# Performance work log

Hardware: AMD Instinct MI355X
Metric: run time of the kernel (lower is better)

Reference implementation:

```python
import jax, jax.numpy as jnp
import numpy as np
import math

B, L, D_MODEL, H = 2, 2048, 2048, 16
HD = D_MODEL // H  # 128


def _rope(x):
    # x: (B,H,L,HD) interleaved-pair RoPE (GPT-NeoX / RoFormer style with ::2 strides)
    hd = x.shape[-1]
    inv_freq = 1.0 / (10000.0 ** (jnp.arange(0, hd, 2, dtype=jnp.float32) / hd))  # (HD/2,)
    t = jnp.arange(x.shape[2], dtype=jnp.float32)
    freqs = t[:, None] * inv_freq[None, :]            # (L, HD/2)
    cos = jnp.cos(freqs)[None, None]                  # (1,1,L,HD/2)
    sin = jnp.sin(freqs)[None, None]
    x1 = x[..., ::2]
    x2 = x[..., 1::2]
    even = x1 * cos - x2 * sin
    odd = x1 * sin + x2 * cos
    # interleave even/odd back: (...,HD/2,2) -> (...,HD)
    return jnp.stack([even, odd], axis=-1).reshape(x.shape)


def setup_inputs() -> dict:
    key = jax.random.key(0)
    k1, k2, k3, k4, k5, k6 = jax.random.split(key, 6)
    x_q = jax.random.normal(k1, (B, L, D_MODEL), dtype=jnp.float32)
    x_kv = jax.random.normal(k2, (B, L, D_MODEL), dtype=jnp.float32)
    # causal additive mask: 0 keep, -1e9 masked, broadcastable to (B,H,L,S)
    causal = jnp.tril(jnp.ones((L, L), dtype=bool))
    attn_mask = jnp.where(causal, 0.0, -1e9).astype(jnp.float32)[None, None]
    s = 0.02
    w_q = jax.random.normal(k3, (D_MODEL, D_MODEL), dtype=jnp.float32) * s
    w_k = jax.random.normal(k4, (D_MODEL, D_MODEL), dtype=jnp.float32) * s
    w_v = jax.random.normal(k5, (D_MODEL, D_MODEL), dtype=jnp.float32) * s
    w_o = jax.random.normal(k6, (D_MODEL, D_MODEL), dtype=jnp.float32) * s
    return {"x_q": x_q, "x_kv": x_kv, "attn_mask": attn_mask,
            "w_q": w_q, "w_k": w_k, "w_v": w_v, "w_o": w_o}


def _shape(x):
    b, l, _ = x.shape
    return x.reshape(b, l, H, HD).transpose(0, 2, 1, 3)  # (B,H,L,HD)


def reference(x_q, x_kv, attn_mask, w_q, w_k, w_v, w_o):
    # torch Linear (no bias): y = x @ W.T
    q = _shape(x_q @ w_q.T)
    k = _shape(x_kv @ w_k.T)
    v = _shape(x_kv @ w_v.T)
    q = _rope(q)
    k = _rope(k)
    scale = 1.0 / math.sqrt(HD)
    scores = jnp.einsum('bhld,bhsd->bhls', q, k) * scale + attn_mask
    attn = jax.nn.softmax(scores, axis=-1)            # (B,H,L,S)
    out = jnp.einsum('bhls,bhsd->bhld', attn, v)
    out = out.transpose(0, 2, 1, 3).reshape(x_q.shape[0], x_q.shape[1], H * HD)
    out = out @ w_o.T
    return (out, attn)
```

## Files before the change

### kernel.cpp

```cpp
#include <hip/hip_runtime.h>
#include <hip/hip_bf16.h>
#include <math.h>

#define B_ 2
#define L_ 2048
#define D_ 2048
#define H_ 16
#define HD_ 128
#define E_ (B_*L_*D_)
#define W_ (D_*D_)

typedef __bf16 bf16;
typedef __bf16 bf16x8 __attribute__((ext_vector_type(8)));
typedef __bf16 bf16x4 __attribute__((ext_vector_type(4)));
typedef float  f32x4  __attribute__((ext_vector_type(4)));

#define GLL16(gp_, lp_) __builtin_amdgcn_global_load_lds( \
    (const __attribute__((address_space(1))) void*)(gp_), \
    (__attribute__((address_space(3))) void*)(lp_), 16, 0, 0)

#define BARRIER() do { asm volatile("" ::: "memory"); \
    __builtin_amdgcn_s_barrier(); \
    asm volatile("" ::: "memory"); } while (0)

#define WAITN(N) asm volatile("s_waitcnt vmcnt(" #N ")" ::: "memory")

__global__ void cvt2(const float* __restrict__ s0, const float* __restrict__ s1,
                     bf16* __restrict__ d0, bf16* __restrict__ d1, int n) {
  const float* s = blockIdx.y ? s1 : s0;
  bf16* d = blockIdx.y ? d1 : d0;
  int i = (blockIdx.x * blockDim.x + threadIdx.x) * 4;
  if (i + 3 < n) {
    f32x4 v = *reinterpret_cast<const f32x4*>(s + i);
    bf16x4 o;
    o[0] = (bf16)v[0]; o[1] = (bf16)v[1]; o[2] = (bf16)v[2]; o[3] = (bf16)v[3];
    *reinterpret_cast<bf16x4*>(d + i) = o;
  }
}
__global__ void cvt4(const float* __restrict__ s0, const float* __restrict__ s1,
                     const float* __restrict__ s2, const float* __restrict__ s3,
                     bf16* __restrict__ d0, bf16* __restrict__ d1,
                     bf16* __restrict__ d2, bf16* __restrict__ d3, int n) {
  const float* s; bf16* d;
  switch (blockIdx.y) {
    case 0: s = s0; d = d0; break;
    case 1: s = s1; d = d1; break;
    case 2: s = s2; d = d2; break;
    default: s = s3; d = d3; break;
  }
  int i = (blockIdx.x * blockDim.x + threadIdx.x) * 4;
  if (i + 3 < n) {
    f32x4 v = *reinterpret_cast<const f32x4*>(s + i);
    bf16x4 o;
    o[0] = (bf16)v[0]; o[1] = (bf16)v[1]; o[2] = (bf16)v[2]; o[3] = (bf16)v[3];
    *reinterpret_cast<bf16x4*>(d + i) = o;
  }
}

__global__ void rope_table(float* __restrict__ ct, float* __restrict__ st) {
  int t = blockIdx.x;
  int i = threadIdx.x;
  float inv = powf(10000.0f, -2.0f * (float)i / 128.0f);
  float f = (float)t * inv;
  ct[t * 64 + i] = cosf(f);
  st[t * 64 + i] = sinf(f);
}

__global__ void rope_inplace(bf16* __restrict__ Q, bf16* __restrict__ Kt,
                             const float* __restrict__ ct, const float* __restrict__ st) {
  size_t idx = (size_t)blockIdx.x * blockDim.x + threadIdx.x;
  const size_t per = E_ / 8;
  bf16* P = (idx < per) ? Q : Kt;
  size_t li = ((idx < per) ? idx : idx - per) * 8;
  int l   = (int)((li / D_) % L_);
  int col = (int)(li % D_);
  int i0  = (col & 127) >> 1;
  bf16x8 v = *reinterpret_cast<const bf16x8*>(P + li);
  f32x4 c4 = *reinterpret_cast<const f32x4*>(ct + l * 64 + i0);
  f32x4 s4 = *reinterpret_cast<const f32x4*>(st + l * 64 + i0);
  bf16x8 o;
#pragma unroll
  for (int p = 0; p < 4; ++p) {
    float x1 = (float)v[2*p], x2 = (float)v[2*p+1];
    o[2*p]   = (bf16)(x1 * c4[p] - x2 * s4[p]);
    o[2*p+1] = (bf16)(x1 * s4[p] + x2 * c4[p]);
  }
  *reinterpret_cast<bf16x8*>(P + li) = o;
}

__global__ void transpose_v(const bf16* __restrict__ Vraw, bf16* __restrict__ Vt) {
  __shared__ bf16 tile[32][33];
  int bh = blockIdx.z; int b = bh >> 4, h = bh & 15;
  int l0 = blockIdx.x * 32, d0 = blockIdx.y * 32;
  int tx = threadIdx.x, ty = threadIdx.y;
#pragma unroll
  for (int j = 0; j < 4; ++j) {
    int r = ty + j * 8;
    tile[r][tx] = Vraw[((size_t)b * L_ + l0 + r) * D_ + h * HD_ + d0 + tx];
  }
  __syncthreads();
#pragma unroll
  for (int j = 0; j < 4; ++j) {
    int r = ty + j * 8;
    Vt[((size_t)bh * HD_ + d0 + r) * L_ + l0 + tx] = tile[tx][r];
  }
}

template<int OUT_BF16>
__global__ __launch_bounds__(256, 4) void gemm_bt(const bf16* __restrict__ A,
                                                  const bf16* __restrict__ Bw,
                                                  void* __restrict__ Cout,
                                                  int M, int N, int K) {
  __shared__ bf16 As[128 * 64];
  __shared__ bf16 Bs[128 * 64];
  const int tid = threadIdx.x;
  const int lane = tid & 63;
  const int w = tid >> 6;
  const int l15 = lane & 15, lg = lane >> 4;
  const int m0 = blockIdx.y * 128, n0 = blockIdx.x * 128;
  const int wm = (w >> 1) * 64, wn = (w & 1) * 64;

  int rowS[4], schS[4];
#pragma unroll
  for (int s = 0; s < 4; ++s) {
    int cl = s * 256 + tid;
    rowS[s] = cl >> 3;
    schS[s] = ((cl & 7) ^ ((cl >> 3) & 7)) << 3;
  }

  f32x4 acc[4][4];
#pragma unroll
  for (int m = 0; m < 4; ++m)
#pragma unroll
    for (int n = 0; n < 4; ++n) acc[m][n] = (f32x4){0.f, 0.f, 0.f, 0.f};

  for (int kt = 0; kt < K; kt += 64) {
    __syncthreads();
#pragma unroll
    for (int s = 0; s < 4; ++s) {
      GLL16(A  + (size_t)(m0 + rowS[s]) * K + kt + schS[s], As + s * 2048 + w * 512);
      GLL16(Bw + (size_t)(n0 + rowS[s]) * K + kt + schS[s], Bs + s * 2048 + w * 512);
    }
    __syncthreads();
#pragma unroll
    for (int kk = 0; kk < 64; kk += 32) {
      bf16x8 af[4], bfr[4];
#pragma unroll
      for (int m = 0; m < 4; ++m)
        af[m] = *reinterpret_cast<const bf16x8*>(
            As + (wm + m * 16 + l15) * 64 + ((((kk >> 3) + lg) ^ (l15 & 7)) << 3));
#pragma unroll
      for (int n = 0; n < 4; ++n)
        bfr[n] = *reinterpret_cast<const bf16x8*>(
            Bs + (wn + n * 16 + l15) * 64 + ((((kk >> 3) + lg) ^ (l15 & 7)) << 3));
#pragma unroll
      for (int m = 0; m < 4; ++m)
#pragma unroll
        for (int n = 0; n < 4; ++n)
          acc[m][n] = __builtin_amdgcn_mfma_f32_16x16x32_bf16(af[m], bfr[n], acc[m][n], 0, 0, 0);
    }
  }
#pragma unroll
  for (int m = 0; m < 4; ++m) {
    int orow = m0 + wm + m * 16 + lg * 4;
#pragma unroll
    for (int n = 0; n < 4; ++n) {
      int col = n0 + wn + n * 16 + l15;
#pragma unroll
      for (int r = 0; r < 4; ++r) {
        if (OUT_BF16) ((bf16*)Cout)[(size_t)(orow + r) * N + col] = (bf16)acc[m][n][r];
        else          ((float*)Cout)[(size_t)(orow + r) * N + col] = acc[m][n][r];
      }
    }
  }
}

__global__ __launch_bounds__(512, 4) void attn_fused(const bf16* __restrict__ Qb,
                                                     const bf16* __restrict__ Kb,
                                                     const bf16* __restrict__ Vt,
                                                     float* __restrict__ attn,
                                                     bf16* __restrict__ Oh) {
  __shared__ bf16 Klds[2][64 * 128];
  __shared__ bf16 Vlds[128 * 64];
  __shared__ bf16 Plds[8][16][72];

  const int tid = threadIdx.x;
  const int w = tid >> 6, lane = tid & 63;
  const int l15 = lane & 15, lg = lane >> 4;

  int g = blockIdx.x + 16 * blockIdx.y;
  int x, bh;
  if (g < 256) { x = g & 15;        bh = g >> 4; }
  else { int h2 = g - 256; x = 15 - (h2 & 15); bh = 16 + (h2 >> 4); }
  const int b = bh >> 4, h = bh & 15;

  const int qt = (w < 4) ? x : (31 - x);
  const int q0w = qt * 64 + (w & 3) * 16;
  const int ntW = qt + 1;
  const int ntB = 32 - x;
  const float sc2 = 0.08838834764831845f * 1.44269504088896f;

  const bf16* kb = Kb + ((size_t)b * L_) * D_ + h * HD_;
  const bf16* vb = Vt + (size_t)bh * HD_ * L_;
  float* arow = attn + ((size_t)bh * L_ + q0w) * L_;

  bf16x8 qf[4];
  {
    const bf16* qrow = Qb + ((size_t)b * L_ + q0w + l15) * D_ + h * HD_;
#pragma unroll
    for (int c = 0; c < 4; ++c)
      qf[c] = *reinterpret_cast<const bf16x8*>(qrow + c * 32 + lg * 8);
  }

  const int t1 = 512 + tid;
  const int rK0 = tid >> 4, sK0 = ((tid & 15) ^ (rK0 & 7)) << 3;
  const int rK1 = t1 >> 4,  sK1 = ((t1 & 15) ^ (rK1 & 7)) << 3;
  const int rV0 = tid >> 3, sV0 = ((tid & 7) ^ (rV0 & 7)) << 3;
  const int rV1 = t1 >> 3,  sV1 = ((t1 & 7) ^ (rV1 & 7)) << 3;
  bf16* ldsK0 = &Klds[0][0] + w * 512;
  bf16* ldsK1 = &Klds[0][0] + 4096 + w * 512;
  bf16* ldsV0 = Vlds + w * 512;
  bf16* ldsV1 = Vlds + 4096 + w * 512;

  auto stageK = [&](int gp, int buf) {
    GLL16(kb + (size_t)(gp * 64 + rK0) * D_ + sK0, ldsK0 + buf * 8192);
    GLL16(kb + (size_t)(gp * 64 + rK1) * D_ + sK1, ldsK1 + buf * 8192);
  };
  auto stageV = [&](int gp) {
    GLL16(vb + (size_t)rV0 * L_ + gp * 64 + sV0, ldsV0);
    GLL16(vb + (size_t)rV1 * L_ + gp * 64 + sV1, ldsV1);
  };
  auto qkt = [&](const bf16* kl, f32x4* acc) {
#pragma unroll
    for (int c = 0; c < 4; ++c)
#pragma unroll
      for (int t = 0; t < 4; ++t) {
        bf16x8 kf = *reinterpret_cast<const bf16x8*>(
            kl + (t * 16 + l15) * 128 + ((((c << 2) + lg) ^ (l15 & 7)) << 3));
        acc[t] = __builtin_amdgcn_mfma_f32_16x16x32_bf16(qf[c], kf, acc[t], 0, 0, 0);
      }
  };

  float sum[4] = {0.f, 0.f, 0.f, 0.f};
  stageK(0, 0);
  for (int gp = 0; gp < ntB; ++gp) {
    BARRIER();
    const bool hn = (gp + 1 < ntB);
    if (hn) stageK(gp + 1, (gp + 1) & 1);
    const bool pz = (gp > 0) && ((gp - 1) >= ntW);
    if (pz) { if (hn) WAITN(18); else WAITN(16); }
    else    { if (hn) WAITN(2);  else WAITN(0);  }
    BARRIER();
    if (gp < ntW) {
      f32x4 acc[4] = {(f32x4){0,0,0,0},(f32x4){0,0,0,0},(f32x4){0,0,0,0},(f32x4){0,0,0,0}};
      qkt(&Klds[gp & 1][0], acc);
      if (gp < qt) {
#pragma unroll
        for (int t = 0; t < 4; ++t)
#pragma unroll
          for (int r = 0; r < 4; ++r)
            sum[r] += exp2f(acc[t][r] * sc2);
      } else {
#pragma unroll
        for (int t = 0; t < 4; ++t)
#pragma unroll
          for (int r = 0; r < 4; ++r) {
            int kc = gp * 64 + t * 16 + l15;
            int qr = q0w + lg * 4 + r;
            sum[r] += (kc <= qr) ? exp2f(acc[t][r] * sc2) : 0.f;
          }
      }
    } else {
#pragma unroll
      for (int t = 0; t < 4; ++t)
#pragma unroll
        for (int r = 0; r < 4; ++r)
          arow[(size_t)(lg * 4 + r) * L_ + gp * 64 + t * 16 + l15] = 0.f;
    }
  }
#pragma unroll
  for (int r = 0; r < 4; ++r) {
#pragma unroll
    for (int sh = 1; sh < 16; sh <<= 1)
      sum[r] += __shfl_xor(sum[r], sh, 64);
  }
  float rinv[4];
#pragma unroll
  for (int r = 0; r < 4; ++r) rinv[r] = 1.0f / sum[r];

  f32x4 oacc[8];
#pragma unroll
  for (int i = 0; i < 8; ++i) oacc[i] = (f32x4){0.f, 0.f, 0.f, 0.f};

  BARRIER();
  stageK(0, 0);
  for (int gp = 0; gp < ntB; ++gp) {
    BARRIER();
    stageV(gp);
    const bool hn = (gp + 1 < ntB);
    if (hn) stageK(gp + 1, (gp + 1) & 1);
    const bool ps = (gp > 0) && ((gp - 1) < ntW);
    if (ps) { if (hn) WAITN(20); else WAITN(18); }
    else    { if (hn) WAITN(4);  else WAITN(2);  }
    BARRIER();
    const bool act = gp < ntW;
    float pv[4][4];
    if (act) {
      f32x4 acc[4] = {(f32x4){0,0,0,0},(f32x4){0,0,0,0},(f32x4){0,0,0,0},(f32x4){0,0,0,0}};
      qkt(&Klds[gp & 1][0], acc);
      if (gp < qt) {
#pragma unroll
        for (int t = 0; t < 4; ++t)
#pragma unroll
          for (int r = 0; r < 4; ++r)
            pv[t][r] = exp2f(acc[t][r] * sc2) * rinv[r];
      } else {
#pragma unroll
        for (int t = 0; t < 4; ++t)
#pragma unroll
          for (int r = 0; r < 4; ++r) {
            int kc = gp * 64 + t * 16 + l15;
            int qr = q0w + lg * 4 + r;
            pv[t][r] = (kc <= qr) ? exp2f(acc[t][r] * sc2) * rinv[r] : 0.f;
          }
      }
#pragma unroll
      for (int t = 0; t < 4; ++t)
#pragma unroll
        for (int r = 0; r < 4; ++r)
          Plds[w][lg * 4 + r][t * 16 + l15] = (bf16)pv[t][r];
    }
    if (hn) WAITN(2); else WAITN(0);
    if (act) {
#pragma unroll
      for (int t = 0; t < 4; ++t)
#pragma unroll
        for (int r = 0; r < 4; ++r)
          arow[(size_t)(lg * 4 + r) * L_ + gp * 64 + t * 16 + l15] = pv[t][r];
    }
    BARRIER();
    if (act) {
      asm volatile("s_waitcnt lgkmcnt(0)" ::: "memory");
      __builtin_amdgcn_sched_barrier(0);
#pragma unroll
      for (int ck = 0; ck < 2; ++ck) {
        bf16x8 pa = *reinterpret_cast<const bf16x8*>(&Plds[w][l15][ck * 32 + lg * 8]);
#pragma unroll
        for (int t8 = 0; t8 < 8; ++t8) {
          bf16x8 vf = *reinterpret_cast<const bf16x8*>(
              Vlds + (t8 * 16 + l15) * 64 + ((((ck << 2) + lg) ^ (l15 & 7)) << 3));
          oacc[t8] = __builtin_amdgcn_mfma_f32_16x16x32_bf16(pa, vf, oacc[t8], 0, 0, 0);
        }
      }
      asm volatile("s_waitcnt lgkmcnt(0)" ::: "memory");
    }
  }

  for (int gp2 = ntB; gp2 < 32; ++gp2) {
#pragma unroll
    for (int it = 0; it < 4; ++it)
      *reinterpret_cast<f32x4*>(arow + (size_t)l15 * L_ + gp2 * 64 + lg * 4 + it * 16)
          = (f32x4){0.f, 0.f, 0.f, 0.f};
  }

  bf16* orow = Oh + ((size_t)b * L_ + q0w) * D_ + h * HD_;
#pragma unroll
  for (int t8 = 0; t8 < 8; ++t8)
#pragma unroll
    for (int r = 0; r < 4; ++r)
      orow[(size_t)(lg * 4 + r) * D_ + t8 * 16 + l15] = (bf16)oacc[t8][r];
}

extern "C" void kernel_launch(void* const* d_in, const int* in_sizes, int n_in,
                              void* d_out, int out_size, void* d_ws, size_t ws_size,
                              hipStream_t stream) {
  const float* x_q  = (const float*)d_in[0];
  const float* x_kv = (const float*)d_in[1];
  const float* w_q = (const float*)d_in[3];
  const float* w_k = (const float*)d_in[4];
  const float* w_v = (const float*)d_in[5];
  const float* w_o = (const float*)d_in[6];

  char* p = (char*)d_ws;
  auto alloc = [&](size_t bytes) { char* r = p; p += (bytes + 255) & ~(size_t)255; return r; };
  bf16* xq_b  = (bf16*)alloc((size_t)E_ * 2);
  bf16* xkv_b = (bf16*)alloc((size_t)E_ * 2);
  bf16* wq_b  = (bf16*)alloc((size_t)W_ * 2);
  bf16* wk_b  = (bf16*)alloc((size_t)W_ * 2);
  bf16* wv_b  = (bf16*)alloc((size_t)W_ * 2);
  bf16* wo_b  = (bf16*)alloc((size_t)W_ * 2);
  bf16* Qraw  = (bf16*)alloc((size_t)E_ * 2);
  bf16* Kraw  = (bf16*)alloc((size_t)E_ * 2);
  bf16* Vraw  = (bf16*)alloc((size_t)E_ * 2);
  bf16* Vt    = (bf16*)alloc((size_t)E_ * 2);
  bf16* Oh    = (bf16*)alloc((size_t)E_ * 2);
  float* ct   = (float*)alloc((size_t)L_ * 64 * 4);
  float* st2  = (float*)alloc((size_t)L_ * 64 * 4);

  float* out0     = (float*)d_out;
  float* attn_out = out0 + E_;

  cvt2<<<dim3(8192, 2), 256, 0, stream>>>(x_q, x_kv, xq_b, xkv_b, E_);
  cvt4<<<dim3(4096, 4), 256, 0, stream>>>(w_q, w_k, w_v, w_o, wq_b, wk_b, wv_b, wo_b, W_);
  rope_table<<<L_, 64, 0, stream>>>(ct, st2);

  gemm_bt<1><<<dim3(16, 32), 256, 0, stream>>>(xq_b,  wq_b, Qraw, B_*L_, D_, D_);
  gemm_bt<1><<<dim3(16, 32), 256, 0, stream>>>(xkv_b, wk_b, Kraw, B_*L_, D_, D_);
  gemm_bt<1><<<dim3(16, 32), 256, 0, stream>>>(xkv_b, wv_b, Vraw, B_*L_, D_, D_);

  rope_inplace<<<8192, 256, 0, stream>>>(Qraw, Kraw, ct, st2);
  transpose_v<<<dim3(64, 4, 32), dim3(32, 8), 0, stream>>>(Vraw, Vt);
  attn_fused<<<dim3(16, 32), 512, 0, stream>>>(Qraw, Kraw, Vt, attn_out, Oh);
  gemm_bt<0><<<dim3(16, 32), 256, 0, stream>>>(Oh, wo_b, out0, B_*L_, D_, D_);
}
```

Baseline: 477.5 us.

## Fuse QKV projections with RoPE and V-transpose epilogues; merge prep kernels

```diff
diff --git a/kernel.cpp b/kernel.cpp
--- a/kernel.cpp
+++ b/kernel.cpp
@@ -25,91 +25,143 @@
 
 #define WAITN(N) asm volatile("s_waitcnt vmcnt(" #N ")" ::: "memory")
 
-__global__ void cvt2(const float* __restrict__ s0, const float* __restrict__ s1,
-                     bf16* __restrict__ d0, bf16* __restrict__ d1, int n) {
-  const float* s = blockIdx.y ? s1 : s0;
-  bf16* d = blockIdx.y ? d1 : d0;
-  int i = (blockIdx.x * blockDim.x + threadIdx.x) * 4;
-  if (i + 3 < n) {
+__global__ void prep(const float* __restrict__ xq, const float* __restrict__ xkv,
+                     const float* __restrict__ wq, const float* __restrict__ wk,
+                     const float* __restrict__ wv, const float* __restrict__ wo,
+                     bf16* __restrict__ xqb, bf16* __restrict__ xkvb,
+                     bf16* __restrict__ wqb, bf16* __restrict__ wkb,
+                     bf16* __restrict__ wvb, bf16* __restrict__ wob,
+                     float* __restrict__ ct, float* __restrict__ st) {
+  int g = blockIdx.x;
+  if (g < 16384) {
+    const float* s = (g < 8192) ? xq : xkv;
+    bf16* d = (g < 8192) ? xqb : xkvb;
+    int i = ((g & 8191) * 256 + threadIdx.x) * 4;
     f32x4 v = *reinterpret_cast<const f32x4*>(s + i);
-    bf16x4 o;
-    o[0] = (bf16)v[0]; o[1] = (bf16)v[1]; o[2] = (bf16)v[2]; o[3] = (bf16)v[3];
+    bf16x4 o; o[0]=(bf16)v[0]; o[1]=(bf16)v[1]; o[2]=(bf16)v[2]; o[3]=(bf16)v[3];
     *reinterpret_cast<bf16x4*>(d + i) = o;
+  } else if (g < 32768) {
+    int gg = g - 16384;
+    int which = gg >> 12;
+    const float* s = (which==0)?wq:(which==1)?wk:(which==2)?wv:wo;
+    bf16* d = (which==0)?wqb:(which==1)?wkb:(which==2)?wvb:wob;
+    int i = ((gg & 4095) * 256 + threadIdx.x) * 4;
+    f32x4 v = *reinterpret_cast<const f32x4*>(s + i);
+    bf16x4 o; o[0]=(bf16)v[0]; o[1]=(bf16)v[1]; o[2]=(bf16)v[2]; o[3]=(bf16)v[3];
+    *reinterpret_cast<bf16x4*>(d + i) = o;
+  } else {
+    int idx = (g - 32768) * 256 + threadIdx.x;
+    int t = idx >> 6, i = idx & 63;
+    float inv = powf(10000.0f, -2.0f * (float)i / 128.0f);
+    float f = (float)t * inv;
+    ct[t * 64 + i] = cosf(f);
+    st[t * 64 + i] = sinf(f);
   }
 }
-__global__ void cvt4(const float* __restrict__ s0, const float* __restrict__ s1,
-                     const float* __restrict__ s2, const float* __restrict__ s3,
-                     bf16* __restrict__ d0, bf16* __restrict__ d1,
-                     bf16* __restrict__ d2, bf16* __restrict__ d3, int n) {
-  const float* s; bf16* d;
-  switch (blockIdx.y) {
-    case 0: s = s0; d = d0; break;
-    case 1: s = s1; d = d1; break;
-    case 2: s = s2; d = d2; break;
-    default: s = s3; d = d3; break;
-  }
-  int i = (blockIdx.x * blockDim.x + threadIdx.x) * 4;
-  if (i + 3 < n) {
-    f32x4 v = *reinterpret_cast<const f32x4*>(s + i);
-    bf16x4 o;
-    o[0] = (bf16)v[0]; o[1] = (bf16)v[1]; o[2] = (bf16)v[2]; o[3] = (bf16)v[3];
-    *reinterpret_cast<bf16x4*>(d + i) = o;
+
+__global__ __launch_bounds__(256, 4) void gemm_qkv(
+    const bf16* __restrict__ xq, const bf16* __restrict__ xkv,
+    const bf16* __restrict__ wq, const bf16* __restrict__ wk, const bf16* __restrict__ wv,
+    const float* __restrict__ ct, const float* __restrict__ st,
+    bf16* __restrict__ Qo, bf16* __restrict__ Ko, bf16* __restrict__ Vt) {
+  __shared__ bf16 As[128 * 64];
+  __shared__ bf16 Bs[128 * 64];
+  const int tid = threadIdx.x;
+  const int lane = tid & 63;
+  const int w = tid >> 6;
+  const int l15 = lane & 15, lg = lane >> 4;
+  const int which = blockIdx.x >> 4;
+  const int n0 = (blockIdx.x & 15) * 128;
+  const int m0 = blockIdx.y * 128;
+  const int wm = (w >> 1) * 64, wn = (w & 1) * 64;
+  const bf16* A  = (which == 0) ? xq : xkv;
+  const bf16* Wt = (which == 0) ? wq : ((which == 1) ? wk : wv);
+
+  int rowS[4], schS[4];
+#pragma unroll
+  for (int s = 0; s < 4; ++s) {
+    int cl = s * 256 + tid;
+    rowS[s] = cl >> 3;
+    schS[s] = ((cl & 7) ^ ((cl >> 3) & 7)) << 3;
+  }
+
+  f32x4 acc[4][4];
+#pragma unroll
+  for (int m = 0; m < 4; ++m)
+#pragma unroll
+    for (int n = 0; n < 4; ++n) acc[m][n] = (f32x4){0.f, 0.f, 0.f, 0.f};
+
+  for (int kt = 0; kt < D_; kt += 64) {
+    __syncthreads();
+#pragma unroll
+    for (int s = 0; s < 4; ++s) {
+      GLL16(A  + (size_t)(m0 + rowS[s]) * D_ + kt + schS[s], As + s * 2048 + w * 512);
+      GLL16(Wt + (size_t)(n0 + rowS[s]) * D_ + kt + schS[s], Bs + s * 2048 + w * 512);
+    }
+    __syncthreads();
+#pragma unroll
+    for (int kk = 0; kk < 64; kk += 32) {
+      bf16x8 af[4], bfr[4];
+#pragma unroll
+      for (int m = 0; m < 4; ++m)
+        af[m] = *reinterpret_cast<const bf16x8*>(
+            As + (wm + m * 16 + l15) * 64 + ((((kk >> 3) + lg) ^ (l15 & 7)) << 3));
+#pragma unroll
+      for (int n = 0; n < 4; ++n)
+        bfr[n] = *reinterpret_cast<const bf16x8*>(
+            Bs + (wn + n * 16 + l15) * 64 + ((((kk >> 3) + lg) ^ (l15 & 7)) << 3));
+#pragma unroll
+      for (int m = 0; m < 4; ++m)
+#pragma unroll
+        for (int n = 0; n < 4; ++n)
+          acc[m][n] = __builtin_amdgcn_mfma_f32_16x16x32_bf16(af[m], bfr[n], acc[m][n], 0, 0, 0);
+    }
+  }
+
+  if (which == 2) {
+    const int b = m0 >> 11;
+    const int l0b = (m0 & 2047) + wm + lg * 4;
+#pragma unroll
+    for (int m = 0; m < 4; ++m) {
+      int l0 = l0b + m * 16;
+#pragma unroll
+      for (int n = 0; n < 4; ++n) {
+        int c = n0 + wn + n * 16 + l15;
+        int hd = (b * 16 + (c >> 7)) * 128 + (c & 127);
+        bf16x4 o;
+        o[0] = (bf16)acc[m][n][0]; o[1] = (bf16)acc[m][n][1];
+        o[2] = (bf16)acc[m][n][2]; o[3] = (bf16)acc[m][n][3];
+        *reinterpret_cast<bf16x4*>(Vt + (size_t)hd * L_ + l0) = o;
+      }
+    }
+  } else {
+    bf16* Out = which ? Ko : Qo;
+    const bool odd = (l15 & 1);
+#pragma unroll
+    for (int m = 0; m < 4; ++m) {
+      int row = m0 + wm + m * 16 + lg * 4;
+      int l = row & 2047;
+#pragma unroll
+      for (int n = 0; n < 4; ++n) {
+        int c = n0 + wn + n * 16 + l15;
+        int i = (c & 127) >> 1;
+#pragma unroll
+        for (int r = 0; r < 4; ++r) {
+          float own = acc[m][n][r];
+          float prt = __shfl_xor(own, 1, 64);
+          float cc = ct[(size_t)(l + r) * 64 + i];
+          float ss = st[(size_t)(l + r) * 64 + i];
+          float res = odd ? (prt * ss + own * cc) : (own * cc - prt * ss);
+          Out[(size_t)(row + r) * D_ + c] = (bf16)res;
+        }
+      }
+    }
   }
 }
 
-__global__ void rope_table(float* __restrict__ ct, float* __restrict__ st) {
-  int t = blockIdx.x;
-  int i = threadIdx.x;
-  float inv = powf(10000.0f, -2.0f * (float)i / 128.0f);
-  float f = (float)t * inv;
-  ct[t * 64 + i] = cosf(f);
-  st[t * 64 + i] = sinf(f);
-}
-
-__global__ void rope_inplace(bf16* __restrict__ Q, bf16* __restrict__ Kt,
-                             const float* __restrict__ ct, const float* __restrict__ st) {
-  size_t idx = (size_t)blockIdx.x * blockDim.x + threadIdx.x;
-  const size_t per = E_ / 8;
-  bf16* P = (idx < per) ? Q : Kt;
-  size_t li = ((idx < per) ? idx : idx - per) * 8;
-  int l   = (int)((li / D_) % L_);
-  int col = (int)(li % D_);
-  int i0  = (col & 127) >> 1;
-  bf16x8 v = *reinterpret_cast<const bf16x8*>(P + li);
-  f32x4 c4 = *reinterpret_cast<const f32x4*>(ct + l * 64 + i0);
-  f32x4 s4 = *reinterpret_cast<const f32x4*>(st + l * 64 + i0);
-  bf16x8 o;
-#pragma unroll
-  for (int p = 0; p < 4; ++p) {
-    float x1 = (float)v[2*p], x2 = (float)v[2*p+1];
-    o[2*p]   = (bf16)(x1 * c4[p] - x2 * s4[p]);
-    o[2*p+1] = (bf16)(x1 * s4[p] + x2 * c4[p]);
-  }
-  *reinterpret_cast<bf16x8*>(P + li) = o;
-}
-
-__global__ void transpose_v(const bf16* __restrict__ Vraw, bf16* __restrict__ Vt) {
-  __shared__ bf16 tile[32][33];
-  int bh = blockIdx.z; int b = bh >> 4, h = bh & 15;
-  int l0 = blockIdx.x * 32, d0 = blockIdx.y * 32;
-  int tx = threadIdx.x, ty = threadIdx.y;
-#pragma unroll
-  for (int j = 0; j < 4; ++j) {
-    int r = ty + j * 8;
-    tile[r][tx] = Vraw[((size_t)b * L_ + l0 + r) * D_ + h * HD_ + d0 + tx];
-  }
-  __syncthreads();
-#pragma unroll
-  for (int j = 0; j < 4; ++j) {
-    int r = ty + j * 8;
-    Vt[((size_t)bh * HD_ + d0 + r) * L_ + l0 + tx] = tile[tx][r];
-  }
-}
-
-template<int OUT_BF16>
 __global__ __launch_bounds__(256, 4) void gemm_bt(const bf16* __restrict__ A,
                                                   const bf16* __restrict__ Bw,
-                                                  void* __restrict__ Cout,
+                                                  float* __restrict__ Cout,
                                                   int M, int N, int K) {
   __shared__ bf16 As[128 * 64];
   __shared__ bf16 Bs[128 * 64];
@@ -167,10 +219,8 @@
     for (int n = 0; n < 4; ++n) {
       int col = n0 + wn + n * 16 + l15;
 #pragma unroll
-      for (int r = 0; r < 4; ++r) {
-        if (OUT_BF16) ((bf16*)Cout)[(size_t)(orow + r) * N + col] = (bf16)acc[m][n][r];
-        else          ((float*)Cout)[(size_t)(orow + r) * N + col] = acc[m][n][r];
-      }
+      for (int r = 0; r < 4; ++r)
+        Cout[(size_t)(orow + r) * N + col] = acc[m][n][r];
     }
   }
 }
@@ -391,7 +441,6 @@
   bf16* wo_b  = (bf16*)alloc((size_t)W_ * 2);
   bf16* Qraw  = (bf16*)alloc((size_t)E_ * 2);
   bf16* Kraw  = (bf16*)alloc((size_t)E_ * 2);
-  bf16* Vraw  = (bf16*)alloc((size_t)E_ * 2);
   bf16* Vt    = (bf16*)alloc((size_t)E_ * 2);
   bf16* Oh    = (bf16*)alloc((size_t)E_ * 2);
   float* ct   = (float*)alloc((size_t)L_ * 64 * 4);
@@ -400,16 +449,10 @@
   float* out0     = (float*)d_out;
   float* attn_out = out0 + E_;
 
-  cvt2<<<dim3(8192, 2), 256, 0, stream>>>(x_q, x_kv, xq_b, xkv_b, E_);
-  cvt4<<<dim3(4096, 4), 256, 0, stream>>>(w_q, w_k, w_v, w_o, wq_b, wk_b, wv_b, wo_b, W_);
-  rope_table<<<L_, 64, 0, stream>>>(ct, st2);
-
-  gemm_bt<1><<<dim3(16, 32), 256, 0, stream>>>(xq_b,  wq_b, Qraw, B_*L_, D_, D_);
-  gemm_bt<1><<<dim3(16, 32), 256, 0, stream>>>(xkv_b, wk_b, Kraw, B_*L_, D_, D_);
-  gemm_bt<1><<<dim3(16, 32), 256, 0, stream>>>(xkv_b, wv_b, Vraw, B_*L_, D_, D_);
-
-  rope_inplace<<<8192, 256, 0, stream>>>(Qraw, Kraw, ct, st2);
-  transpose_v<<<dim3(64, 4, 32), dim3(32, 8), 0, stream>>>(Vraw, Vt);
+  prep<<<33280, 256, 0, stream>>>(x_q, x_kv, w_q, w_k, w_v, w_o,
+                                  xq_b, xkv_b, wq_b, wk_b, wv_b, wo_b, ct, st2);
+  gemm_qkv<<<dim3(48, 32), 256, 0, stream>>>(xq_b, xkv_b, wq_b, wk_b, wv_b,
+                                             ct, st2, Qraw, Kraw, Vt);
   attn_fused<<<dim3(16, 32), 512, 0, stream>>>(Qraw, Kraw, Vt, attn_out, Oh);
-  gemm_bt<0><<<dim3(16, 32), 256, 0, stream>>>(Oh, wo_b, out0, B_*L_, D_, D_);
+  gemm_bt<<<dim3(16, 32), 256, 0, stream>>>(Oh, wo_b, out0, B_*L_, D_, D_);
 }
```

After: 446.2 us. 1.07x faster.
